# Kernel tuning notes

Measured on AMD Instinct MI355X. Metric: run time of the kernel, lower is better.

Reference implementation:

```python
import jax, jax.numpy as jnp
import numpy as np

D = 1024        # hidden_dim
E = 8           # num_experts
K = 2           # activated_experts
H = 4 * D       # ffn hidden


def setup_inputs() -> dict:
    key = jax.random.key(0)
    ks = jax.random.split(key, 12)
    s = 1.0 / np.sqrt(D)
    sh = 1.0 / np.sqrt(H)
    return {
        "x": jax.random.normal(ks[0], (2, 2048, D), dtype=jnp.float32),
        "gate_w": jax.random.uniform(ks[1], (D, E), minval=-s, maxval=s, dtype=jnp.float32),
        "gate_b": jax.random.uniform(ks[2], (E,), minval=-s, maxval=s, dtype=jnp.float32),
        "route_bias": jnp.zeros((E,), dtype=jnp.float32),
        "shared_w1": jax.random.uniform(ks[3], (D, H), minval=-s, maxval=s, dtype=jnp.float32),
        "shared_b1": jax.random.uniform(ks[4], (H,), minval=-s, maxval=s, dtype=jnp.float32),
        "shared_w2": jax.random.uniform(ks[5], (H, D), minval=-sh, maxval=sh, dtype=jnp.float32),
        "shared_b2": jax.random.uniform(ks[6], (D,), minval=-sh, maxval=sh, dtype=jnp.float32),
        "exp_w1": jax.random.uniform(ks[7], (E, D, H), minval=-s, maxval=s, dtype=jnp.float32),
        "exp_b1": jax.random.uniform(ks[8], (E, H), minval=-s, maxval=s, dtype=jnp.float32),
        "exp_w2": jax.random.uniform(ks[9], (E, H, D), minval=-sh, maxval=sh, dtype=jnp.float32),
        "exp_b2": jax.random.uniform(ks[10], (E, D), minval=-sh, maxval=sh, dtype=jnp.float32),
    }


def reference(x, gate_w, gate_b, route_bias, shared_w1, shared_b1, shared_w2,
              shared_b2, exp_w1, exp_b1, exp_w2, exp_b2):
    B, S, _ = x.shape
    xf = x.reshape(-1, D)                                  # [T, D]
    T = xf.shape[0]

    # Routing: gate logits + learned load-balancing bias -> softmax -> top-k
    gate_logits = xf @ gate_w + gate_b + route_bias        # [T, E]
    gate_probs = jax.nn.softmax(gate_logits, axis=-1)
    topk_p, topk_i = jax.lax.top_k(gate_probs, K)          # [T, K]
    topk_p = topk_p / jnp.sum(topk_p, axis=-1, keepdims=True)

    # Per-token combine weights over experts (zero for unselected experts)
    w = jnp.zeros((T, E), dtype=xf.dtype)
    w = w.at[jnp.arange(T)[:, None], topk_i].add(topk_p)   # [T, E]

    # Dense per-expert FFN (grouped GEMM form), weighted combine
    h = jax.nn.gelu(jnp.einsum('td,edh->eth', xf, exp_w1) + exp_b1[:, None, :],
                    approximate=False)                     # [E, T, H]
    y = jnp.einsum('eth,ehd->etd', h, exp_w2) + exp_b2[:, None, :]  # [E, T, D]
    combined = jnp.einsum('etd,te->td', y, w)              # [T, D]

    # Shared expert
    sh = jax.nn.gelu(xf @ shared_w1 + shared_b1, approximate=False)
    shared_out = sh @ shared_w2 + shared_b2                # [T, D]

    return (shared_out + combined).reshape(B, S, D)
```

## Files before the change

kernel.cpp:

```cpp
#include <hip/hip_runtime.h>
#include <math.h>

#define TT 4096
#define DD 1024
#define EE 8
#define HH 4096
#define NEXP 9
#define NTMAX 104
#define NSG 13

typedef __bf16 bf16;
typedef __bf16 bf16x8 __attribute__((ext_vector_type(8)));
typedef float  f32x4  __attribute__((ext_vector_type(4)));

#define GLOAD_LDS16(gptr, lptr)                                                   \
  __builtin_amdgcn_global_load_lds(                                               \
      (const __attribute__((address_space(1))) void*)(gptr),                      \
      (__attribute__((address_space(3))) void*)(lptr), 16, 0, 0)

__global__ void k_init(const float* __restrict__ x, bf16* __restrict__ xb,
                       float* __restrict__ out, int* __restrict__ counts,
                       int* __restrict__ cursors) {
  int i = blockIdx.x * blockDim.x + threadIdx.x;
  if (i < TT * DD) { xb[i] = (bf16)x[i]; out[i] = 0.0f; }
  if (i < EE) { counts[i] = 0; cursors[i] = 0; }
}

__global__ void k_route(const float* __restrict__ x, const float* __restrict__ gw,
                        const float* __restrict__ gb, const float* __restrict__ rb,
                        int* __restrict__ counts, int* __restrict__ tke,
                        float* __restrict__ tkp) {
  int gid = blockIdx.x * blockDim.x + threadIdx.x;
  int t = gid >> 6;
  int lane = gid & 63;
  if (t >= TT) return;
  const float* xt = x + (size_t)t * DD;
  float acc[EE];
#pragma unroll
  for (int e = 0; e < EE; e++) acc[e] = 0.f;
  for (int d = lane; d < DD; d += 64) {
    float xv = xt[d];
    const float* g = gw + (size_t)d * EE;
#pragma unroll
    for (int e = 0; e < EE; e++) acc[e] += xv * g[e];
  }
#pragma unroll
  for (int off = 32; off > 0; off >>= 1) {
#pragma unroll
    for (int e = 0; e < EE; e++) acc[e] += __shfl_down(acc[e], off);
  }
  if (lane == 0) {
    float l[EE];
#pragma unroll
    for (int e = 0; e < EE; e++) l[e] = acc[e] + gb[e] + rb[e];
    int i1 = 0;
#pragma unroll
    for (int e = 1; e < EE; e++) if (l[e] > l[i1]) i1 = e;
    int i2 = (i1 == 0) ? 1 : 0;
#pragma unroll
    for (int e = 0; e < EE; e++) if (e != i1 && l[e] > l[i2]) i2 = e;
    float e2 = expf(l[i2] - l[i1]);
    float s = 1.f + e2;
    tke[t * 2 + 0] = i1; tkp[t * 2 + 0] = 1.f / s;
    tke[t * 2 + 1] = i2; tkp[t * 2 + 1] = e2 / s;
    atomicAdd(&counts[i1], 1);
    atomicAdd(&counts[i2], 1);
  }
}

__global__ void k_prefix(const int* __restrict__ counts, int* __restrict__ expBase,
                         int* __restrict__ expCnt, int* __restrict__ tileExp,
                         int* __restrict__ tileM, int* __restrict__ nTiles) {
  if (blockIdx.x == 0 && threadIdx.x == 0) {
    int off = TT;
    for (int e = 0; e < EE; e++) { expBase[e] = off; expCnt[e] = counts[e]; off += counts[e]; }
    expBase[8] = 0; expCnt[8] = TT;
    int idx = 0;
    for (int mt = 0; mt < TT / 128; mt++) { tileExp[idx] = 8; tileM[idx] = mt; idx++; }
    for (int e = 0; e < EE; e++) {
      int nt = (counts[e] + 127) >> 7;
      for (int mt = 0; mt < nt; mt++) { tileExp[idx] = e; tileM[idx] = mt; idx++; }
    }
    *nTiles = idx;
  }
}

__global__ void k_scatter(const int* __restrict__ tke, const float* __restrict__ tkp,
                          const int* __restrict__ expBase, int* __restrict__ cursors,
                          int* __restrict__ rowTok, float* __restrict__ rowW) {
  int t = blockIdx.x * blockDim.x + threadIdx.x;
  if (t >= TT) return;
  rowTok[t] = t; rowW[t] = 1.f;
#pragma unroll
  for (int k = 0; k < 2; k++) {
    int e = tke[t * 2 + k];
    float p = tkp[t * 2 + k];
    int slot = atomicAdd(&cursors[e], 1);
    int r = expBase[e] + slot;
    rowTok[r] = t; rowW[r] = p;
  }
}

__global__ __launch_bounds__(256) void k_wt(const float* __restrict__ expW,
                                            const float* __restrict__ shW,
                                            bf16* __restrict__ outT, int K, int N) {
  __shared__ float t[64][65];
  int z = blockIdx.z;
  const float* W = (z == 8) ? shW : expW + (size_t)z * K * N;
  bf16* O = outT + (size_t)z * K * N;
  int n0 = blockIdx.x * 64, k0 = blockIdx.y * 64;
  int tid = threadIdx.x;
  int kr = tid >> 2;
  int cf = (tid & 3) * 16;
#pragma unroll
  for (int i = 0; i < 4; i++) {
    f32x4 v = *(const f32x4*)&W[(size_t)(k0 + kr) * N + n0 + cf + i * 4];
    t[kr][cf + i * 4 + 0] = v[0];
    t[kr][cf + i * 4 + 1] = v[1];
    t[kr][cf + i * 4 + 2] = v[2];
    t[kr][cf + i * 4 + 3] = v[3];
  }
  __syncthreads();
  int nr = tid >> 2;
  int kf = (tid & 3) * 16;
  bf16x8 o0, o1;
#pragma unroll
  for (int j = 0; j < 8; j++) o0[j] = (bf16)t[kf + j][nr];
#pragma unroll
  for (int j = 0; j < 8; j++) o1[j] = (bf16)t[kf + 8 + j][nr];
  bf16* dst = O + (size_t)(n0 + nr) * K + k0 + kf;
  *(bf16x8*)dst = o0;
  *(bf16x8*)(dst + 8) = o1;
}

__global__ __launch_bounds__(256, 2) void k_gemm1(
    const bf16* __restrict__ xb, const bf16* __restrict__ wt1,
    const float* __restrict__ sb1, const float* __restrict__ eb1,
    const int* __restrict__ rowTok, const int* __restrict__ expBase,
    const int* __restrict__ expCnt, const int* __restrict__ tileExp,
    const int* __restrict__ tileM, const int* __restrict__ nTiles,
    bf16* __restrict__ hbuf) {
  int bid = blockIdx.x;
  int sg  = bid >> 8;
  int rem = bid & 255;
  int n   = rem >> 3;
  int dm  = rem & 7;
  int tIdx = sg * 8 + dm;
  if (tIdx >= *nTiles) return;
  int ex = tileExp[tIdx];
  int mt = tileM[tIdx];
  int base = expBase[ex];
  int cnt  = expCnt[ex];
  int n0 = n * 128;
  const bf16* Bt = wt1 + (size_t)ex * HH * DD;
  const float* b1 = (ex == 8) ? sb1 : eb1 + (size_t)ex * HH;

  __shared__ bf16 As[128 * 32];
  __shared__ bf16 Bs[128 * 32];
  __shared__ int  toks[128];

  int tid = threadIdx.x;
  int lane = tid & 63;
  int wv = tid >> 6;
  int wm = (wv & 1) * 64;
  int wn = (wv >> 1) * 64;

  if (tid < 128) {
    int rr = min(mt * 128 + tid, cnt - 1);
    toks[tid] = rowTok[base + rr];
  }

  f32x4 acc[4][4];
#pragma unroll
  for (int a = 0; a < 4; a++)
#pragma unroll
    for (int b = 0; b < 4; b++) acc[a][b] = (f32x4){0.f, 0.f, 0.f, 0.f};

  __syncthreads();

  int r0 = wv * 32 + (lane >> 2);
  int c8 = (lane & 3) * 8;

  for (int k0 = 0; k0 < DD; k0 += 32) {
    GLOAD_LDS16(xb + (size_t)toks[r0] * DD + k0 + c8,      As + wv * 1024);
    GLOAD_LDS16(xb + (size_t)toks[r0 + 16] * DD + k0 + c8, As + wv * 1024 + 512);
    GLOAD_LDS16(Bt + (size_t)(n0 + r0) * DD + k0 + c8,      Bs + wv * 1024);
    GLOAD_LDS16(Bt + (size_t)(n0 + r0 + 16) * DD + k0 + c8, Bs + wv * 1024 + 512);
    __syncthreads();
    bf16x8 af[4], bfr[4];
#pragma unroll
    for (int mi = 0; mi < 4; mi++)
      af[mi] = *(const bf16x8*)&As[(wm + mi * 16 + (lane & 15)) * 32 + (lane >> 4) * 8];
#pragma unroll
    for (int ni = 0; ni < 4; ni++)
      bfr[ni] = *(const bf16x8*)&Bs[(wn + ni * 16 + (lane & 15)) * 32 + (lane >> 4) * 8];
#pragma unroll
    for (int mi = 0; mi < 4; mi++)
#pragma unroll
      for (int ni = 0; ni < 4; ni++)
        acc[mi][ni] = __builtin_amdgcn_mfma_f32_16x16x32_bf16(af[mi], bfr[ni], acc[mi][ni], 0, 0, 0);
    __syncthreads();
  }

  int rsub = (lane >> 4) * 4;
#pragma unroll
  for (int ni = 0; ni < 4; ni++) {
    int col = n0 + wn + ni * 16 + (lane & 15);
    float bias = b1[col];
#pragma unroll
    for (int mi = 0; mi < 4; mi++) {
#pragma unroll
      for (int r = 0; r < 4; r++) {
        int mrow = mt * 128 + wm + mi * 16 + rsub + r;
        if (mrow < cnt) {
          float v = acc[mi][ni][r] + bias;
          v = 0.5f * v * (1.f + erff(v * 0.70710678118654752f));
          hbuf[(size_t)(base + mrow) * HH + col] = (bf16)v;
        }
      }
    }
  }
}

__global__ __launch_bounds__(256, 2) void k_gemm2(
    const bf16* __restrict__ hbuf, const bf16* __restrict__ wt2,
    const float* __restrict__ sb2, const float* __restrict__ eb2,
    const int* __restrict__ rowTok, const float* __restrict__ rowW,
    const int* __restrict__ expBase, const int* __restrict__ expCnt,
    const int* __restrict__ tileExp, const int* __restrict__ tileM,
    const int* __restrict__ nTiles, float* __restrict__ out) {
  int bid = blockIdx.x;
  int sg  = bid >> 6;
  int rem = bid & 63;
  int n   = rem >> 3;
  int dm  = rem & 7;
  int tIdx = sg * 8 + dm;
  if (tIdx >= *nTiles) return;
  int ex = tileExp[tIdx];
  int mt = tileM[tIdx];
  int base = expBase[ex];
  int cnt  = expCnt[ex];
  int n0 = n * 128;
  const bf16* Bt = wt2 + (size_t)ex * DD * HH;
  const float* b2 = (ex == 8) ? sb2 : eb2 + (size_t)ex * DD;

  __shared__ bf16 As[128 * 32];
  __shared__ bf16 Bs[128 * 32];
  __shared__ int   toks[128];
  __shared__ float wrow[128];

  int tid = threadIdx.x;
  int lane = tid & 63;
  int wv = tid >> 6;
  int wm = (wv & 1) * 64;
  int wn = (wv >> 1) * 64;

  if (tid < 128) {
    int rr = min(mt * 128 + tid, cnt - 1);
    toks[tid] = rowTok[base + rr];
    wrow[tid] = rowW[base + rr];
  }

  f32x4 acc[4][4];
#pragma unroll
  for (int a = 0; a < 4; a++)
#pragma unroll
    for (int b = 0; b < 4; b++) acc[a][b] = (f32x4){0.f, 0.f, 0.f, 0.f};

  __syncthreads();

  int r0 = wv * 32 + (lane >> 2);
  int c8 = (lane & 3) * 8;
  int pr0 = base + min(mt * 128 + r0, cnt - 1);
  int pr1 = base + min(mt * 128 + r0 + 16, cnt - 1);
  const bf16* ga0 = hbuf + (size_t)pr0 * HH + c8;
  const bf16* ga1 = hbuf + (size_t)pr1 * HH + c8;

  for (int k0 = 0; k0 < HH; k0 += 32) {
    GLOAD_LDS16(ga0 + k0, As + wv * 1024);
    GLOAD_LDS16(ga1 + k0, As + wv * 1024 + 512);
    GLOAD_LDS16(Bt + (size_t)(n0 + r0) * HH + k0 + c8,      Bs + wv * 1024);
    GLOAD_LDS16(Bt + (size_t)(n0 + r0 + 16) * HH + k0 + c8, Bs + wv * 1024 + 512);
    __syncthreads();
    bf16x8 af[4], bfr[4];
#pragma unroll
    for (int mi = 0; mi < 4; mi++)
      af[mi] = *(const bf16x8*)&As[(wm + mi * 16 + (lane & 15)) * 32 + (lane >> 4) * 8];
#pragma unroll
    for (int ni = 0; ni < 4; ni++)
      bfr[ni] = *(const bf16x8*)&Bs[(wn + ni * 16 + (lane & 15)) * 32 + (lane >> 4) * 8];
#pragma unroll
    for (int mi = 0; mi < 4; mi++)
#pragma unroll
      for (int ni = 0; ni < 4; ni++)
        acc[mi][ni] = __builtin_amdgcn_mfma_f32_16x16x32_bf16(af[mi], bfr[ni], acc[mi][ni], 0, 0, 0);
    __syncthreads();
  }

  int rsub = (lane >> 4) * 4;
#pragma unroll
  for (int ni = 0; ni < 4; ni++) {
    int col = n0 + wn + ni * 16 + (lane & 15);
    float bias = b2[col];
#pragma unroll
    for (int mi = 0; mi < 4; mi++) {
#pragma unroll
      for (int r = 0; r < 4; r++) {
        int local = wm + mi * 16 + rsub + r;
        int mrow = mt * 128 + local;
        if (mrow < cnt) {
          float v = acc[mi][ni][r] + bias;
          atomicAdd(&out[(size_t)toks[local] * DD + col], wrow[local] * v);
        }
      }
    }
  }
}

extern "C" void kernel_launch(void* const* d_in, const int* in_sizes, int n_in,
                              void* d_out, int out_size, void* d_ws, size_t ws_size,
                              hipStream_t stream) {
  const float* x   = (const float*)d_in[0];
  const float* gw  = (const float*)d_in[1];
  const float* gb  = (const float*)d_in[2];
  const float* rb  = (const float*)d_in[3];
  const float* sw1 = (const float*)d_in[4];
  const float* sb1 = (const float*)d_in[5];
  const float* sw2 = (const float*)d_in[6];
  const float* sb2 = (const float*)d_in[7];
  const float* ew1 = (const float*)d_in[8];
  const float* eb1 = (const float*)d_in[9];
  const float* ew2 = (const float*)d_in[10];
  const float* eb2 = (const float*)d_in[11];
  float* out = (float*)d_out;

  char* p = (char*)d_ws;
  bf16* xb    = (bf16*)p;  p += (size_t)TT * DD * sizeof(bf16);
  bf16* hbuf  = (bf16*)p;  p += (size_t)(3 * TT) * HH * sizeof(bf16);
  bf16* wtb   = (bf16*)p;  p += (size_t)NEXP * DD * HH * sizeof(bf16);
  int* rowTok = (int*)p;   p += (size_t)(3 * TT) * sizeof(int);
  float* rowW = (float*)p; p += (size_t)(3 * TT) * sizeof(float);
  int* tke    = (int*)p;   p += (size_t)TT * 2 * sizeof(int);
  float* tkp  = (float*)p; p += (size_t)TT * 2 * sizeof(float);
  int* counts = (int*)p;   p += EE * sizeof(int);
  int* cursors= (int*)p;   p += EE * sizeof(int);
  int* expBase= (int*)p;   p += NEXP * sizeof(int);
  int* expCnt = (int*)p;   p += NEXP * sizeof(int);
  int* tileExp= (int*)p;   p += 128 * sizeof(int);
  int* tileM  = (int*)p;   p += 128 * sizeof(int);
  int* nTiles = (int*)p;   p += 8 * sizeof(int);

  k_init<<<(TT * DD + 255) / 256, 256, 0, stream>>>(x, xb, out, counts, cursors);
  k_route<<<TT / 4, 256, 0, stream>>>(x, gw, gb, rb, counts, tke, tkp);
  k_prefix<<<1, 64, 0, stream>>>(counts, expBase, expCnt, tileExp, tileM, nTiles);
  k_scatter<<<TT / 256, 256, 0, stream>>>(tke, tkp, expBase, cursors, rowTok, rowW);

  dim3 gt1(HH / 64, DD / 64, NEXP);
  k_wt<<<gt1, 256, 0, stream>>>(ew1, sw1, wtb, DD, HH);
  k_gemm1<<<NSG * 8 * (HH / 128), 256, 0, stream>>>(xb, wtb, sb1, eb1, rowTok, expBase,
                                                    expCnt, tileExp, tileM, nTiles, hbuf);

  dim3 gt2(DD / 64, HH / 64, NEXP);
  k_wt<<<gt2, 256, 0, stream>>>(ew2, sw2, wtb, HH, DD);
  k_gemm2<<<NSG * 8 * (DD / 128), 256, 0, stream>>>(hbuf, wtb, sb2, eb2, rowTok, rowW,
                                                    expBase, expCnt, tileExp, tileM, nTiles, out);
}
```

Before: 904.5 us.

## Swizzle LDS GEMM tiles, stage GELU epilogue through LDS, use tanh GELU

```diff
diff --git a/kernel.cpp b/kernel.cpp
--- a/kernel.cpp
+++ b/kernel.cpp
@@ -132,6 +132,7 @@
   *(bf16x8*)dst = o0;
   *(bf16x8*)(dst + 8) = o1;
 }
+
 
 __global__ __launch_bounds__(256, 2) void k_gemm1(
     const bf16* __restrict__ xb, const bf16* __restrict__ wt1,
@@ -179,7 +180,8 @@
   __syncthreads();
 
   int r0 = wv * 32 + (lane >> 2);
-  int c8 = (lane & 3) * 8;
+  int c8 = ((lane & 3) ^ ((lane >> 3) & 3)) * 8;
+  int fsw = (((lane >> 4) ^ ((lane >> 1) & 3)) * 8);
 
   for (int k0 = 0; k0 < DD; k0 += 32) {
     GLOAD_LDS16(xb + (size_t)toks[r0] * DD + k0 + c8,      As + wv * 1024);
@@ -190,10 +192,10 @@
     bf16x8 af[4], bfr[4];
 #pragma unroll
     for (int mi = 0; mi < 4; mi++)
-      af[mi] = *(const bf16x8*)&As[(wm + mi * 16 + (lane & 15)) * 32 + (lane >> 4) * 8];
+      af[mi] = *(const bf16x8*)&As[(wm + mi * 16 + (lane & 15)) * 32 + fsw];
 #pragma unroll
     for (int ni = 0; ni < 4; ni++)
-      bfr[ni] = *(const bf16x8*)&Bs[(wn + ni * 16 + (lane & 15)) * 32 + (lane >> 4) * 8];
+      bfr[ni] = *(const bf16x8*)&Bs[(wn + ni * 16 + (lane & 15)) * 32 + fsw];
 #pragma unroll
     for (int mi = 0; mi < 4; mi++)
 #pragma unroll
@@ -202,22 +204,37 @@
     __syncthreads();
   }
 
+  bf16* T = ((wv & 2) ? Bs : As) + (wv & 1) * 1024;
+  int colL = lane & 15;
   int rsub = (lane >> 4) * 4;
-#pragma unroll
-  for (int ni = 0; ni < 4; ni++) {
-    int col = n0 + wn + ni * 16 + (lane & 15);
-    float bias = b1[col];
-#pragma unroll
-    for (int mi = 0; mi < 4; mi++) {
+  float bs[4];
+#pragma unroll
+  for (int ni = 0; ni < 4; ni++) bs[ni] = b1[n0 + wn + ni * 16 + colL];
+  for (int mi = 0; mi < 4; mi++) {
+#pragma unroll
+    for (int ni = 0; ni < 4; ni++) {
 #pragma unroll
       for (int r = 0; r < 4; r++) {
-        int mrow = mt * 128 + wm + mi * 16 + rsub + r;
-        if (mrow < cnt) {
-          float v = acc[mi][ni][r] + bias;
-          v = 0.5f * v * (1.f + erff(v * 0.70710678118654752f));
-          hbuf[(size_t)(base + mrow) * HH + col] = (bf16)v;
-        }
+        float v = acc[mi][ni][r] + bs[ni];
+        float u = 1.5957691f * v * (1.f + 0.044715f * v * v);
+        v = v / (1.f + __expf(-u));
+        int qrow = rsub + r;
+        int col = ni * 16 + colL;
+        int chp = (col >> 3) ^ (qrow & 7);
+        T[qrow * 64 + chp * 8 + (col & 7)] = (bf16)v;
       }
+    }
+    int rr = lane >> 2;
+    int cb = (lane & 3) * 16;
+    int ch0 = ((cb >> 3) + 0) ^ (rr & 7);
+    int ch1 = ((cb >> 3) + 1) ^ (rr & 7);
+    bf16x8 o0 = *(bf16x8*)&T[rr * 64 + ch0 * 8];
+    bf16x8 o1 = *(bf16x8*)&T[rr * 64 + ch1 * 8];
+    int mrow = mt * 128 + wm + mi * 16 + rr;
+    if (mrow < cnt) {
+      bf16* dst = hbuf + (size_t)(base + mrow) * HH + n0 + wn + cb;
+      *(bf16x8*)dst = o0;
+      *(bf16x8*)(dst + 8) = o1;
     }
   }
 }
@@ -270,7 +287,8 @@
   __syncthreads();
 
   int r0 = wv * 32 + (lane >> 2);
-  int c8 = (lane & 3) * 8;
+  int c8 = ((lane & 3) ^ ((lane >> 3) & 3)) * 8;
+  int fsw = (((lane >> 4) ^ ((lane >> 1) & 3)) * 8);
   int pr0 = base + min(mt * 128 + r0, cnt - 1);
   int pr1 = base + min(mt * 128 + r0 + 16, cnt - 1);
   const bf16* ga0 = hbuf + (size_t)pr0 * HH + c8;
@@ -285,10 +303,10 @@
     bf16x8 af[4], bfr[4];
 #pragma unroll
     for (int mi = 0; mi < 4; mi++)
-      af[mi] = *(const bf16x8*)&As[(wm + mi * 16 + (lane & 15)) * 32 + (lane >> 4) * 8];
+      af[mi] = *(const bf16x8*)&As[(wm + mi * 16 + (lane & 15)) * 32 + fsw];
 #pragma unroll
     for (int ni = 0; ni < 4; ni++)
-      bfr[ni] = *(const bf16x8*)&Bs[(wn + ni * 16 + (lane & 15)) * 32 + (lane >> 4) * 8];
+      bfr[ni] = *(const bf16x8*)&Bs[(wn + ni * 16 + (lane & 15)) * 32 + fsw];
 #pragma unroll
     for (int mi = 0; mi < 4; mi++)
 #pragma unroll
```

After: 859.6 us. 1.05x faster.
